# Performance work log

Measured on AMD Instinct MI355X. Metric: run time of the kernel, lower is better.

The kernel has to match this reference:

```python
import jax, jax.numpy as jnp
import numpy as np

T, B, S = 32, 32, 64
I = H = C = 1024  # input_size == hidden_size required by the original module's wiring
A = 128           # attention_size


def setup_inputs() -> dict:
    key = jax.random.key(0)
    ks = jax.random.split(key, 10)
    s_ih = 1.0 / np.sqrt(H)
    s_a = 1.0 / np.sqrt(H + C)
    return {
        "inputs": jax.random.normal(ks[0], (T, B, I), jnp.float32),
        "context": jax.random.normal(ks[1], (S, B, C), jnp.float32),
        # LSTMCell params (PyTorch layout: gates ordered i, f, g, o)
        "W_ih": jax.random.normal(ks[2], (4 * H, I), jnp.float32) * s_ih,
        "W_hh": jax.random.normal(ks[3], (4 * H, H), jnp.float32) * s_ih,
        "b_ih": jax.random.normal(ks[4], (4 * H,), jnp.float32) * s_ih,
        "b_hh": jax.random.normal(ks[5], (4 * H,), jnp.float32) * s_ih,
        # Attention params: linear1 [A, H+C], linear2 [1, A]
        "W1": jax.random.normal(ks[6], (A, H + C), jnp.float32) * s_a,
        "b1": jax.random.normal(ks[7], (A,), jnp.float32) * s_a,
        "W2": jax.random.normal(ks[8], (1, A), jnp.float32) * (1.0 / np.sqrt(A)),
        "b2": jax.random.normal(ks[9], (1,), jnp.float32) * (1.0 / np.sqrt(A)),
    }


def reference(inputs, context, W_ih, W_hh, b_ih, b_hh, W1, b1, W2, b2):
    Tn, Bn, _ = inputs.shape
    Hn = W_hh.shape[1]
    xt = jnp.transpose(context, (1, 0, 2))  # [B, S, C]
    # Split linear1 weight into hidden-part and context-part so the
    # context projection can be hoisted out of the time loop (same math
    # as concatenating [y, xt] then applying linear1).
    W1_y = W1[:, :Hn]          # [A, H]
    W1_x = W1[:, Hn:]          # [A, C]
    ctx_proj = jnp.einsum('bsc,ac->bsa', xt, W1_x)  # [B, S, A]
    bias = b_ih + b_hh

    def step(carry, x_t):
        h, c = carry
        gates = x_t @ W_ih.T + h @ W_hh.T + bias   # [B, 4H]
        i, f, g, o = jnp.split(gates, 4, axis=-1)
        c_new = jax.nn.sigmoid(f) * c + jax.nn.sigmoid(i) * jnp.tanh(g)
        h_new = jax.nn.sigmoid(o) * jnp.tanh(c_new)
        # additive attention: linear1 (no nonlinearity in original) -> linear2 -> softmax
        hid = h_new[:, None, :] @ W1_y.T[None] + ctx_proj + b1  # [B, S, A]
        scores = jnp.einsum('bsa,a->bs', hid, W2[0]) + b2[0]    # [B, S]
        attn = jax.nn.softmax(scores, axis=-1)
        weighted = jnp.einsum('bs,bsc->bc', attn, xt)           # [B, C]
        return (h_new, c_new), (weighted, attn)

    h0 = jnp.zeros((Bn, Hn), inputs.dtype)
    (h, c), (outputs, attentions) = jax.lax.scan(step, (h0, h0), inputs)
    return outputs, h, c, attentions
```

## Files before the change

kernel.cpp:

```cpp
#include <hip/hip_runtime.h>

#define T_ 32
#define B_ 32
#define S_ 64
#define C_ 1024
#define H_ 1024
#define NWG 64
#define HSLOT 32768

typedef __attribute__((ext_vector_type(8))) short bf16x8;
typedef __attribute__((ext_vector_type(4))) float f32x4;

#define OUT_H   1048576
#define OUT_CC  1081344
#define OUT_AT  1114112

__device__ __forceinline__ ushort f2b(float f) {
  unsigned u = __float_as_uint(f);
  unsigned r = (u + 0x7FFFu + ((u >> 16) & 1u)) >> 16;
  return (ushort)r;
}
__device__ __forceinline__ float b2f(ushort h) {
  return __uint_as_float(((unsigned)h) << 16);
}

__global__ __launch_bounds__(256) void k_init(const float* __restrict__ inp, ushort* __restrict__ inpb,
                                              const float* __restrict__ Wih, ushort* __restrict__ Wihb,
                                              const float* __restrict__ Whh, ushort* __restrict__ Whhb,
                                              const float* __restrict__ W1, const float* __restrict__ W2,
                                              const float* __restrict__ bih, const float* __restrict__ bhh,
                                              float* __restrict__ v, float* __restrict__ bias,
                                              ushort* __restrict__ hring, unsigned* __restrict__ flags) {
  int blk = blockIdx.x, tid = threadIdx.x;
  if (blk < 4608) {
    const float* src; ushort* dst; int base;
    if (blk < 512) { src = inp; dst = inpb; base = blk; }
    else if (blk < 2560) { src = Wih; dst = Wihb; base = blk - 512; }
    else { src = Whh; dst = Whhb; base = blk - 2560; }
    size_t i = ((size_t)base * 256 + tid) * 8;
    float4 v0 = *reinterpret_cast<const float4*>(src + i);
    float4 v1 = *reinterpret_cast<const float4*>(src + i + 4);
    uint4 o;
    o.x = (unsigned)f2b(v0.x) | ((unsigned)f2b(v0.y) << 16);
    o.y = (unsigned)f2b(v0.z) | ((unsigned)f2b(v0.w) << 16);
    o.z = (unsigned)f2b(v1.x) | ((unsigned)f2b(v1.y) << 16);
    o.w = (unsigned)f2b(v1.z) | ((unsigned)f2b(v1.w) << 16);
    *reinterpret_cast<uint4*>(dst + i) = o;
  } else if (blk < 4612) {
    int c = (blk - 4608) * 256 + tid;
    float acc = 0.f;
#pragma unroll 8
    for (int a = 0; a < 128; ++a) acc += W1[a * 2048 + 1024 + c] * W2[a];
    v[c] = acc;
  } else if (blk < 4628) {
    int jj = (blk - 4612) * 256 + tid;
    bias[jj] = bih[jj] + bhh[jj];
  } else if (blk < 4632) {
    unsigned* hz = reinterpret_cast<unsigned*>(hring);
    int base = (blk - 4628) * 4096;
    for (int i = 0; i < 16; ++i) hz[base + i * 256 + tid] = 0u;
  } else {
    for (int i = 0; i < 4; ++i) flags[i * 256 + tid] = 0u;
  }
}

__global__ __launch_bounds__(256) void k_attn(const float* __restrict__ ctx, const float* __restrict__ v,
                                              float* __restrict__ wgt, float* __restrict__ out) {
  int b = blockIdx.x, tid = threadIdx.x;
  int lane = tid & 63, w = tid >> 6;
  __shared__ float v_s[1024];
  __shared__ float sc_s[64];
  __shared__ float att_s[64];
  for (int i = 0; i < 4; ++i) v_s[tid + i * 256] = v[tid + i * 256];
  __syncthreads();
  for (int si = 0; si < 16; ++si) {
    int s = w * 16 + si;
    const float* xr = ctx + (size_t)(s * B_ + b) * C_;
    float acc = 0.f;
#pragma unroll
    for (int i = 0; i < 16; ++i) { int c = lane + i * 64; acc += xr[c] * v_s[c]; }
    for (int off = 32; off; off >>= 1) acc += __shfl_down(acc, off);
    if (lane == 0) sc_s[s] = acc;
  }
  __syncthreads();
  if (tid < 64) {
    float val = sc_s[tid];
    float mx = val;
    for (int off = 32; off; off >>= 1) mx = fmaxf(mx, __shfl_xor(mx, off));
    float e = expf(val - mx);
    float sm = e;
    for (int off = 32; off; off >>= 1) sm += __shfl_xor(sm, off);
    att_s[tid] = e / sm;
  }
  __syncthreads();
  const float4* ctx4 = reinterpret_cast<const float4*>(ctx);
  float4 a4 = {0.f, 0.f, 0.f, 0.f};
  for (int s = 0; s < 64; ++s) {
    float a = att_s[s];
    float4 x = ctx4[(size_t)(s * B_ + b) * 256 + tid];
    a4.x += a * x.x; a4.y += a * x.y; a4.z += a * x.z; a4.w += a * x.w;
  }
  reinterpret_cast<float4*>(wgt + b * 1024)[tid] = a4;
  if (tid < 64) {
    float av = att_s[tid];
#pragma unroll 4
    for (int t = 0; t < T_; ++t) out[OUT_AT + (t * B_ + b) * 64 + tid] = av;
  }
}

__global__ __launch_bounds__(1024, 4) void k_rec(const ushort* __restrict__ Whhb, const ushort* __restrict__ Wihb,
                                                 const ushort* __restrict__ inpb, ushort* __restrict__ hring,
                                                 const float* __restrict__ wgt, const float* __restrict__ bias,
                                                 float* __restrict__ out, unsigned* __restrict__ flags) {
  int tid = threadIdx.x, lane = tid & 63, w = tid >> 6;
  int wg = blockIdx.x;
  int q = w & 3, ks = w >> 2;
  int g = lane >> 4, r = lane & 15;
  int hidx0 = wg * 16 + q * 4;
  int kbase = ks * 256;
  int j = (r >> 2) * 1024 + hidx0 + (r & 3);
  bf16x8 ah[8], ax[8];
  {
    const ushort* ap = Whhb + (size_t)j * 1024 + kbase + g * 8;
    const ushort* axp = Wihb + (size_t)j * 1024 + kbase + g * 8;
#pragma unroll
    for (int kk = 0; kk < 8; ++kk) {
      ah[kk] = *reinterpret_cast<const bf16x8*>(ap + kk * 32);
      ax[kk] = *reinterpret_cast<const bf16x8*>(axp + kk * 32);
    }
  }
  __shared__ uint4 hl4[4096];
  __shared__ float red[4][4][16][32];
  __shared__ __align__(16) ushort hs[32][16];
  float c_reg = 0.f;
  int eb = tid & 31, hl = (tid >> 5) & 3, qq = tid >> 7;
  int ehidx = wg * 16 + qq * 4 + hl;
  float bs_i = 0.f, bs_f = 0.f, bs_g = 0.f, bs_o = 0.f;
  if (tid < 512) {
    bs_i = bias[ehidx];
    bs_f = bias[1024 + ehidx];
    bs_g = bias[2048 + ehidx];
    bs_o = bias[3072 + ehidx];
  }
  int cb = ks * 32 + g;

#pragma unroll 1
  for (int t = 0; t < T_; ++t) {
    {
      const uint4* s4 = reinterpret_cast<const uint4*>(inpb + (size_t)t * HSLOT);
      uint4 v0 = s4[tid], v1 = s4[tid + 1024], v2 = s4[tid + 2048], v3 = s4[tid + 3072];
      int c0 = tid, c1 = tid + 1024, c2 = tid + 2048, c3 = tid + 3072;
      hl4[(c0 >> 7) * 128 + ((c0 & 127) ^ ((c0 >> 7) & 7))] = v0;
      hl4[(c1 >> 7) * 128 + ((c1 & 127) ^ ((c1 >> 7) & 7))] = v1;
      hl4[(c2 >> 7) * 128 + ((c2 & 127) ^ ((c2 >> 7) & 7))] = v2;
      hl4[(c3 >> 7) * 128 + ((c3 & 127) ^ ((c3 >> 7) & 7))] = v3;
    }
    __syncthreads();
    f32x4 acc0 = (f32x4)(0.f), acc1 = (f32x4)(0.f);
#pragma unroll
    for (int kk = 0; kk < 8; ++kk) {
      int c16 = cb + kk * 4;
      bf16x8 b0 = *reinterpret_cast<const bf16x8*>(&hl4[r * 128 + (c16 ^ (r & 7))]);
      bf16x8 b1 = *reinterpret_cast<const bf16x8*>(&hl4[(r + 16) * 128 + (c16 ^ (r & 7))]);
      acc0 = __builtin_amdgcn_mfma_f32_16x16x32_bf16(ax[kk], b0, acc0, 0, 0, 0);
      acc1 = __builtin_amdgcn_mfma_f32_16x16x32_bf16(ax[kk], b1, acc1, 0, 0, 0);
    }
    if (t > 0 && w == 0) {
      for (;;) {
        unsigned vfl = __hip_atomic_load(&flags[lane * 16], __ATOMIC_RELAXED, __HIP_MEMORY_SCOPE_AGENT);
        if (__all((int)(vfl >= (unsigned)t))) break;
        __builtin_amdgcn_s_sleep(1);
      }
    }
    __syncthreads();
    {
      const uint4* s4 = reinterpret_cast<const uint4*>(hring + (size_t)t * HSLOT);
      uint4 v0 = s4[tid], v1 = s4[tid + 1024], v2 = s4[tid + 2048], v3 = s4[tid + 3072];
      int c0 = tid, c1 = tid + 1024, c2 = tid + 2048, c3 = tid + 3072;
      hl4[(c0 >> 7) * 128 + ((c0 & 127) ^ ((c0 >> 7) & 7))] = v0;
      hl4[(c1 >> 7) * 128 + ((c1 & 127) ^ ((c1 >> 7) & 7))] = v1;
      hl4[(c2 >> 7) * 128 + ((c2 & 127) ^ ((c2 >> 7) & 7))] = v2;
      hl4[(c3 >> 7) * 128 + ((c3 & 127) ^ ((c3 >> 7) & 7))] = v3;
    }
    __syncthreads();
#pragma unroll
    for (int kk = 0; kk < 8; ++kk) {
      int c16 = cb + kk * 4;
      bf16x8 b0 = *reinterpret_cast<const bf16x8*>(&hl4[r * 128 + (c16 ^ (r & 7))]);
      bf16x8 b1 = *reinterpret_cast<const bf16x8*>(&hl4[(r + 16) * 128 + (c16 ^ (r & 7))]);
      acc0 = __builtin_amdgcn_mfma_f32_16x16x32_bf16(ah[kk], b0, acc0, 0, 0, 0);
      acc1 = __builtin_amdgcn_mfma_f32_16x16x32_bf16(ah[kk], b1, acc1, 0, 0, 0);
    }
#pragma unroll
    for (int e = 0; e < 4; ++e) {
      red[q][ks][g * 4 + e][r] = acc0[e];
      red[q][ks][g * 4 + e][r + 16] = acc1[e];
    }
    __syncthreads();
    if (tid < 512) {
      float ig = red[qq][0][0 + hl][eb]  + red[qq][1][0 + hl][eb]  + red[qq][2][0 + hl][eb]  + red[qq][3][0 + hl][eb]  + bs_i;
      float fg = red[qq][0][4 + hl][eb]  + red[qq][1][4 + hl][eb]  + red[qq][2][4 + hl][eb]  + red[qq][3][4 + hl][eb]  + bs_f;
      float gg = red[qq][0][8 + hl][eb]  + red[qq][1][8 + hl][eb]  + red[qq][2][8 + hl][eb]  + red[qq][3][8 + hl][eb]  + bs_g;
      float og = red[qq][0][12 + hl][eb] + red[qq][1][12 + hl][eb] + red[qq][2][12 + hl][eb] + red[qq][3][12 + hl][eb] + bs_o;
      float si = 1.f / (1.f + __expf(-ig));
      float sf = 1.f / (1.f + __expf(-fg));
      float so = 1.f / (1.f + __expf(-og));
      float c_new = sf * c_reg + si * tanhf(gg);
      float h_new = so * tanhf(c_new);
      c_reg = c_new;
      hs[eb][qq * 4 + hl] = f2b(h_new);
      if (t == T_ - 1) {
        out[OUT_H + eb * 1024 + ehidx] = h_new;
        out[OUT_CC + eb * 1024 + ehidx] = c_new;
      }
    }
    __syncthreads();
    if (t != T_ - 1 && w == 0) {
      ushort* hout = hring + (size_t)(t + 1) * HSLOT;
      int b = lane >> 1, half = lane & 1;
      uint4 vv = *reinterpret_cast<const uint4*>(&hs[b][half * 8]);
      unsigned* hp = reinterpret_cast<unsigned*>(hout) + b * 512 + wg * 8 + half * 4;
      __hip_atomic_store(hp + 0, vv.x, __ATOMIC_RELAXED, __HIP_MEMORY_SCOPE_AGENT);
      __hip_atomic_store(hp + 1, vv.y, __ATOMIC_RELAXED, __HIP_MEMORY_SCOPE_AGENT);
      __hip_atomic_store(hp + 2, vv.z, __ATOMIC_RELAXED, __HIP_MEMORY_SCOPE_AGENT);
      __hip_atomic_store(hp + 3, vv.w, __ATOMIC_RELAXED, __HIP_MEMORY_SCOPE_AGENT);
      asm volatile("s_waitcnt vmcnt(0)" ::: "memory");
      if (lane == 0)
        __hip_atomic_store(&flags[wg * 16], (unsigned)(t + 1), __ATOMIC_RELAXED, __HIP_MEMORY_SCOPE_AGENT);
    }
    if (tid >= 512 && tid < 640) {
      int lcl = tid - 512;
      int off = ((wg & 1) << 9) + (lcl << 2);
      float4 vv = *reinterpret_cast<const float4*>(wgt + ((wg >> 1) << 10) + off);
      *reinterpret_cast<float4*>(out + ((size_t)(t * 32 + (wg >> 1)) << 10) + off) = vv;
    }
  }
}

extern "C" void kernel_launch(void* const* d_in, const int* in_sizes, int n_in,
                              void* d_out, int out_size, void* d_ws, size_t ws_size,
                              hipStream_t stream) {
  const float* inp = (const float*)d_in[0];
  const float* ctx = (const float*)d_in[1];
  const float* Wih = (const float*)d_in[2];
  const float* Whh = (const float*)d_in[3];
  const float* bih = (const float*)d_in[4];
  const float* bhh = (const float*)d_in[5];
  const float* W1  = (const float*)d_in[6];
  const float* W2  = (const float*)d_in[8];
  float* out = (float*)d_out;
  char* wsb = (char*)d_ws;

  float* v     = (float*)(wsb + 0);
  float* bias  = (float*)(wsb + 4096);
  float* wgt   = (float*)(wsb + 20480);
  ushort* hring = (ushort*)(wsb + 151552);
  ushort* inpb = (ushort*)(wsb + 2314240);
  ushort* Wihb = (ushort*)(wsb + 4411392);
  ushort* Whhb = (ushort*)(wsb + 12800000);
  unsigned* flags = (unsigned*)(wsb + 21188608);

  hipLaunchKernelGGL(k_init, dim3(4633), dim3(256), 0, stream,
                     inp, inpb, Wih, Wihb, Whh, Whhb, W1, W2, bih, bhh, v, bias, hring, flags);
  hipLaunchKernelGGL(k_attn, dim3(32), dim3(256), 0, stream, ctx, v, wgt, out);

  const ushort* Whhb_c = Whhb;
  const ushort* Wihb_c = Wihb;
  const ushort* inpb_c = inpb;
  const float* wgt_c = wgt;
  const float* bias_c = bias;
  void* kargs[8];
  kargs[0] = (void*)&Whhb_c;
  kargs[1] = (void*)&Wihb_c;
  kargs[2] = (void*)&inpb_c;
  kargs[3] = (void*)&hring;
  kargs[4] = (void*)&wgt_c;
  kargs[5] = (void*)&bias_c;
  kargs[6] = (void*)&out;
  kargs[7] = (void*)&flags;
  hipLaunchCooperativeKernel((const void*)k_rec, dim3(NWG), dim3(1024), kargs, 0, stream);
}
```

Measured before the change: 217.7 us.

## Fuse input and recurrent GEMMs via concatenated weights, LDS atomic reduction

Concatenates W_ih and W_hh into one [4H, 2H] bf16 matrix so each wave does a single K=512 MFMA chain over [x_t, h_t] staged together in LDS. The split-K reduction now uses LDS atomicAdd into a double-buffered accumulator instead of summing four partials. The weighted-context output is written for every timestep directly by the attention kernel instead of by the recurrent kernel. The cost is that the x_t @ W_ih product, which used to run before the spin-wait and overlap it, now sits on the critical path after the barrier. The change also adds LDS atomic contention and uses twice the LDS buffer.

```diff
diff --git a/kernel.cpp b/kernel.cpp
--- a/kernel.cpp
+++ b/kernel.cpp
@@ -25,19 +25,29 @@
 }
 
 __global__ __launch_bounds__(256) void k_init(const float* __restrict__ inp, ushort* __restrict__ inpb,
-                                              const float* __restrict__ Wih, ushort* __restrict__ Wihb,
-                                              const float* __restrict__ Whh, ushort* __restrict__ Whhb,
+                                              const float* __restrict__ Wih, const float* __restrict__ Whh,
+                                              ushort* __restrict__ Wcat,
                                               const float* __restrict__ W1, const float* __restrict__ W2,
                                               const float* __restrict__ bih, const float* __restrict__ bhh,
                                               float* __restrict__ v, float* __restrict__ bias,
                                               ushort* __restrict__ hring, unsigned* __restrict__ flags) {
   int blk = blockIdx.x, tid = threadIdx.x;
-  if (blk < 4608) {
-    const float* src; ushort* dst; int base;
-    if (blk < 512) { src = inp; dst = inpb; base = blk; }
-    else if (blk < 2560) { src = Wih; dst = Wihb; base = blk - 512; }
-    else { src = Whh; dst = Whhb; base = blk - 2560; }
+  if (blk < 512) {
+    size_t i = ((size_t)blk * 256 + tid) * 8;
+    float4 v0 = *reinterpret_cast<const float4*>(inp + i);
+    float4 v1 = *reinterpret_cast<const float4*>(inp + i + 4);
+    uint4 o;
+    o.x = (unsigned)f2b(v0.x) | ((unsigned)f2b(v0.y) << 16);
+    o.y = (unsigned)f2b(v0.z) | ((unsigned)f2b(v0.w) << 16);
+    o.z = (unsigned)f2b(v1.x) | ((unsigned)f2b(v1.y) << 16);
+    o.w = (unsigned)f2b(v1.z) | ((unsigned)f2b(v1.w) << 16);
+    *reinterpret_cast<uint4*>(inpb + i) = o;
+  } else if (blk < 4608) {
+    const float* src = (blk < 2560) ? Wih : Whh;
+    int base = (blk < 2560) ? (blk - 512) : (blk - 2560);
+    int koff = (blk < 2560) ? 0 : 1024;
     size_t i = ((size_t)base * 256 + tid) * 8;
+    int j = (int)(i >> 10), k = (int)(i & 1023);
     float4 v0 = *reinterpret_cast<const float4*>(src + i);
     float4 v1 = *reinterpret_cast<const float4*>(src + i + 4);
     uint4 o;
@@ -45,7 +55,7 @@
     o.y = (unsigned)f2b(v0.z) | ((unsigned)f2b(v0.w) << 16);
     o.z = (unsigned)f2b(v1.x) | ((unsigned)f2b(v1.y) << 16);
     o.w = (unsigned)f2b(v1.z) | ((unsigned)f2b(v1.w) << 16);
-    *reinterpret_cast<uint4*>(dst + i) = o;
+    *reinterpret_cast<uint4*>(Wcat + (size_t)j * 2048 + koff + k) = o;
   } else if (blk < 4612) {
     int c = (blk - 4608) * 256 + tid;
     float acc = 0.f;
@@ -65,7 +75,7 @@
 }
 
 __global__ __launch_bounds__(256) void k_attn(const float* __restrict__ ctx, const float* __restrict__ v,
-                                              float* __restrict__ wgt, float* __restrict__ out) {
+                                              float* __restrict__ out) {
   int b = blockIdx.x, tid = threadIdx.x;
   int lane = tid & 63, w = tid >> 6;
   __shared__ float v_s[1024];
@@ -100,7 +110,9 @@
     float4 x = ctx4[(size_t)(s * B_ + b) * 256 + tid];
     a4.x += a * x.x; a4.y += a * x.y; a4.z += a * x.z; a4.w += a * x.w;
   }
-  reinterpret_cast<float4*>(wgt + b * 1024)[tid] = a4;
+#pragma unroll 4
+  for (int t = 0; t < T_; ++t)
+    reinterpret_cast<float4*>(out + (size_t)(t * B_ + b) * C_)[tid] = a4;
   if (tid < 64) {
     float av = att_s[tid];
 #pragma unroll 4
@@ -108,29 +120,22 @@
   }
 }
 
-__global__ __launch_bounds__(1024, 4) void k_rec(const ushort* __restrict__ Whhb, const ushort* __restrict__ Wihb,
-                                                 const ushort* __restrict__ inpb, ushort* __restrict__ hring,
-                                                 const float* __restrict__ wgt, const float* __restrict__ bias,
+__global__ __launch_bounds__(1024, 4) void k_rec(const ushort* __restrict__ Wcat, const ushort* __restrict__ inpb,
+                                                 ushort* __restrict__ hring, const float* __restrict__ bias,
                                                  float* __restrict__ out, unsigned* __restrict__ flags) {
   int tid = threadIdx.x, lane = tid & 63, w = tid >> 6;
   int wg = blockIdx.x;
   int q = w & 3, ks = w >> 2;
   int g = lane >> 4, r = lane & 15;
-  int hidx0 = wg * 16 + q * 4;
-  int kbase = ks * 256;
-  int j = (r >> 2) * 1024 + hidx0 + (r & 3);
-  bf16x8 ah[8], ax[8];
+  int j = (r >> 2) * 1024 + wg * 16 + q * 4 + (r & 3);
+  bf16x8 a[16];
   {
-    const ushort* ap = Whhb + (size_t)j * 1024 + kbase + g * 8;
-    const ushort* axp = Wihb + (size_t)j * 1024 + kbase + g * 8;
-#pragma unroll
-    for (int kk = 0; kk < 8; ++kk) {
-      ah[kk] = *reinterpret_cast<const bf16x8*>(ap + kk * 32);
-      ax[kk] = *reinterpret_cast<const bf16x8*>(axp + kk * 32);
-    }
-  }
-  __shared__ uint4 hl4[4096];
-  __shared__ float red[4][4][16][32];
+    const ushort* ap = Wcat + (size_t)j * 2048 + ks * 512 + g * 8;
+#pragma unroll
+    for (int kk = 0; kk < 16; ++kk) a[kk] = *reinterpret_cast<const bf16x8*>(ap + kk * 32);
+  }
+  __shared__ uint4 buf[8192];
+  __shared__ float red[2][4][16][32];
   __shared__ __align__(16) ushort hs[32][16];
   float c_reg = 0.f;
   int eb = tid & 31, hl = (tid >> 5) & 3, qq = tid >> 7;
@@ -142,29 +147,17 @@
     bs_g = bias[2048 + ehidx];
     bs_o = bias[3072 + ehidx];
   }
-  int cb = ks * 32 + g;
+  int c16s = tid & 255, rowb = tid >> 8;
+  int swz_w[8];
+#pragma unroll
+  for (int i = 0; i < 8; ++i) {
+    int row = rowb + i * 4;
+    swz_w[i] = row * 256 + (c16s ^ (row & 7));
+  }
 
 #pragma unroll 1
   for (int t = 0; t < T_; ++t) {
-    {
-      const uint4* s4 = reinterpret_cast<const uint4*>(inpb + (size_t)t * HSLOT);
-      uint4 v0 = s4[tid], v1 = s4[tid + 1024], v2 = s4[tid + 2048], v3 = s4[tid + 3072];
-      int c0 = tid, c1 = tid + 1024, c2 = tid + 2048, c3 = tid + 3072;
-      hl4[(c0 >> 7) * 128 + ((c0 & 127) ^ ((c0 >> 7) & 7))] = v0;
-      hl4[(c1 >> 7) * 128 + ((c1 & 127) ^ ((c1 >> 7) & 7))] = v1;
-      hl4[(c2 >> 7) * 128 + ((c2 & 127) ^ ((c2 >> 7) & 7))] = v2;
-      hl4[(c3 >> 7) * 128 + ((c3 & 127) ^ ((c3 >> 7) & 7))] = v3;
-    }
-    __syncthreads();
-    f32x4 acc0 = (f32x4)(0.f), acc1 = (f32x4)(0.f);
-#pragma unroll
-    for (int kk = 0; kk < 8; ++kk) {
-      int c16 = cb + kk * 4;
-      bf16x8 b0 = *reinterpret_cast<const bf16x8*>(&hl4[r * 128 + (c16 ^ (r & 7))]);
-      bf16x8 b1 = *reinterpret_cast<const bf16x8*>(&hl4[(r + 16) * 128 + (c16 ^ (r & 7))]);
-      acc0 = __builtin_amdgcn_mfma_f32_16x16x32_bf16(ax[kk], b0, acc0, 0, 0, 0);
-      acc1 = __builtin_amdgcn_mfma_f32_16x16x32_bf16(ax[kk], b1, acc1, 0, 0, 0);
-    }
+    int p = t & 1;
     if (t > 0 && w == 0) {
       for (;;) {
         unsigned vfl = __hip_atomic_load(&flags[lane * 16], __ATOMIC_RELAXED, __HIP_MEMORY_SCOPE_AGENT);
@@ -174,34 +167,46 @@
     }
     __syncthreads();
     {
-      const uint4* s4 = reinterpret_cast<const uint4*>(hring + (size_t)t * HSLOT);
-      uint4 v0 = s4[tid], v1 = s4[tid + 1024], v2 = s4[tid + 2048], v3 = s4[tid + 3072];
-      int c0 = tid, c1 = tid + 1024, c2 = tid + 2048, c3 = tid + 3072;
-      hl4[(c0 >> 7) * 128 + ((c0 & 127) ^ ((c0 >> 7) & 7))] = v0;
-      hl4[(c1 >> 7) * 128 + ((c1 & 127) ^ ((c1 >> 7) & 7))] = v1;
-      hl4[(c2 >> 7) * 128 + ((c2 & 127) ^ ((c2 >> 7) & 7))] = v2;
-      hl4[(c3 >> 7) * 128 + ((c3 & 127) ^ ((c3 >> 7) & 7))] = v3;
-    }
-    __syncthreads();
-#pragma unroll
-    for (int kk = 0; kk < 8; ++kk) {
+      float* z = &red[p ^ 1][0][0][0];
+      z[tid] = 0.f; z[tid + 1024] = 0.f;
+      if (t == 0) {
+        float* z0 = &red[0][0][0][0];
+        z0[tid] = 0.f; z0[tid + 1024] = 0.f;
+      }
+    }
+    {
+      const ushort* xsrc = inpb + (size_t)t * HSLOT;
+      const ushort* hsrc = hring + (size_t)t * HSLOT;
+      const ushort* colb = (c16s < 128) ? (xsrc + c16s * 8) : (hsrc + (c16s - 128) * 8);
+#pragma unroll
+      for (int i = 0; i < 8; ++i) {
+        int row = rowb + i * 4;
+        buf[swz_w[i]] = *reinterpret_cast<const uint4*>(colb + (size_t)row * 1024);
+      }
+    }
+    __syncthreads();
+    f32x4 acc0 = (f32x4)(0.f), acc1 = (f32x4)(0.f);
+    int cb = ks * 64 + g;
+#pragma unroll
+    for (int kk = 0; kk < 16; ++kk) {
       int c16 = cb + kk * 4;
-      bf16x8 b0 = *reinterpret_cast<const bf16x8*>(&hl4[r * 128 + (c16 ^ (r & 7))]);
-      bf16x8 b1 = *reinterpret_cast<const bf16x8*>(&hl4[(r + 16) * 128 + (c16 ^ (r & 7))]);
-      acc0 = __builtin_amdgcn_mfma_f32_16x16x32_bf16(ah[kk], b0, acc0, 0, 0, 0);
-      acc1 = __builtin_amdgcn_mfma_f32_16x16x32_bf16(ah[kk], b1, acc1, 0, 0, 0);
+      int x0 = r * 256 + (c16 ^ (r & 7));
+      bf16x8 b0 = *reinterpret_cast<const bf16x8*>(&buf[x0]);
+      bf16x8 b1 = *reinterpret_cast<const bf16x8*>(&buf[x0 + 16 * 256]);
+      acc0 = __builtin_amdgcn_mfma_f32_16x16x32_bf16(a[kk], b0, acc0, 0, 0, 0);
+      acc1 = __builtin_amdgcn_mfma_f32_16x16x32_bf16(a[kk], b1, acc1, 0, 0, 0);
     }
 #pragma unroll
     for (int e = 0; e < 4; ++e) {
-      red[q][ks][g * 4 + e][r] = acc0[e];
-      red[q][ks][g * 4 + e][r + 16] = acc1[e];
+      atomicAdd(&red[p][q][g * 4 + e][r], acc0[e]);
+      atomicAdd(&red[p][q][g * 4 + e][r + 16], acc1[e]);
     }
     __syncthreads();
     if (tid < 512) {
-      float ig = red[qq][0][0 + hl][eb]  + red[qq][1][0 + hl][eb]  + red[qq][2][0 + hl][eb]  + red[qq][3][0 + hl][eb]  + bs_i;
-      float fg = red[qq][0][4 + hl][eb]  + red[qq][1][4 + hl][eb]  + red[qq][2][4 + hl][eb]  + red[qq][3][4 + hl][eb]  + bs_f;
-      float gg = red[qq][0][8 + hl][eb]  + red[qq][1][8 + hl][eb]  + red[qq][2][8 + hl][eb]  + red[qq][3][8 + hl][eb]  + bs_g;
-      float og = red[qq][0][12 + hl][eb] + red[qq][1][12 + hl][eb] + red[qq][2][12 + hl][eb] + red[qq][3][12 + hl][eb] + bs_o;
+      float ig = red[p][qq][0 + hl][eb]  + bs_i;
+      float fg = red[p][qq][4 + hl][eb]  + bs_f;
+      float gg = red[p][qq][8 + hl][eb]  + bs_g;
+      float og = red[p][qq][12 + hl][eb] + bs_o;
       float si = 1.f / (1.f + __expf(-ig));
       float sf = 1.f / (1.f + __expf(-fg));
       float so = 1.f / (1.f + __expf(-og));
@@ -227,12 +232,6 @@
       asm volatile("s_waitcnt vmcnt(0)" ::: "memory");
       if (lane == 0)
         __hip_atomic_store(&flags[wg * 16], (unsigned)(t + 1), __ATOMIC_RELAXED, __HIP_MEMORY_SCOPE_AGENT);
-    }
-    if (tid >= 512 && tid < 640) {
-      int lcl = tid - 512;
-      int off = ((wg & 1) << 9) + (lcl << 2);
-      float4 vv = *reinterpret_cast<const float4*>(wgt + ((wg >> 1) << 10) + off);
-      *reinterpret_cast<float4*>(out + ((size_t)(t * 32 + (wg >> 1)) << 10) + off) = vv;
     }
   }
 }
@@ -253,30 +252,24 @@
 
   float* v     = (float*)(wsb + 0);
   float* bias  = (float*)(wsb + 4096);
-  float* wgt   = (float*)(wsb + 20480);
-  ushort* hring = (ushort*)(wsb + 151552);
-  ushort* inpb = (ushort*)(wsb + 2314240);
-  ushort* Wihb = (ushort*)(wsb + 4411392);
-  ushort* Whhb = (ushort*)(wsb + 12800000);
-  unsigned* flags = (unsigned*)(wsb + 21188608);
+  ushort* hring = (ushort*)(wsb + 32768);
+  ushort* inpb = (ushort*)(wsb + 2195456);
+  ushort* Wcat = (ushort*)(wsb + 4292608);
+  unsigned* flags = (unsigned*)(wsb + 21069824);
 
   hipLaunchKernelGGL(k_init, dim3(4633), dim3(256), 0, stream,
-                     inp, inpb, Wih, Wihb, Whh, Whhb, W1, W2, bih, bhh, v, bias, hring, flags);
-  hipLaunchKernelGGL(k_attn, dim3(32), dim3(256), 0, stream, ctx, v, wgt, out);
-
-  const ushort* Whhb_c = Whhb;
-  const ushort* Wihb_c = Wihb;
+                     inp, inpb, Wih, Whh, Wcat, W1, W2, bih, bhh, v, bias, hring, flags);
+  hipLaunchKernelGGL(k_attn, dim3(32), dim3(256), 0, stream, ctx, v, out);
+
+  const ushort* Wcat_c = Wcat;
   const ushort* inpb_c = inpb;
-  const float* wgt_c = wgt;
   const float* bias_c = bias;
-  void* kargs[8];
-  kargs[0] = (void*)&Whhb_c;
-  kargs[1] = (void*)&Wihb_c;
-  kargs[2] = (void*)&inpb_c;
-  kargs[3] = (void*)&hring;
-  kargs[4] = (void*)&wgt_c;
-  kargs[5] = (void*)&bias_c;
-  kargs[6] = (void*)&out;
-  kargs[7] = (void*)&flags;
+  void* kargs[6];
+  kargs[0] = (void*)&Wcat_c;
+  kargs[1] = (void*)&inpb_c;
+  kargs[2] = (void*)&hring;
+  kargs[3] = (void*)&bias_c;
+  kargs[4] = (void*)&out;
+  kargs[5] = (void*)&flags;
   hipLaunchCooperativeKernel((const void*)k_rec, dim3(NWG), dim3(1024), kargs, 0, stream);
 }
```

New measurement: 593.8 us. +172.7%, slower.

## Fuse attention kernel into cooperative recurrent kernel as extra workgroups

Applied to the files above, without the earlier changes.

Removes the separate attention launch by adding 32 extra workgroups to the cooperative recurrent kernel that compute the attention scores, softmax and weighted context per batch and write outputs directly for all timesteps. The recurrent workgroups no longer copy the weighted vector into the output each step. This saves one kernel launch and runs attention concurrently with the recurrence. In exchange it adds more LDS per block and more workgroups that must be co-resident for the cooperative launch.

```diff
diff --git a/kernel.cpp b/kernel.cpp
--- a/kernel.cpp
+++ b/kernel.cpp
@@ -64,56 +64,68 @@
   }
 }
 
-__global__ __launch_bounds__(256) void k_attn(const float* __restrict__ ctx, const float* __restrict__ v,
-                                              float* __restrict__ wgt, float* __restrict__ out) {
-  int b = blockIdx.x, tid = threadIdx.x;
-  int lane = tid & 63, w = tid >> 6;
+__global__ __launch_bounds__(1024, 4) void k_rec(const ushort* __restrict__ Whhb, const ushort* __restrict__ Wihb,
+                                                 const ushort* __restrict__ inpb, ushort* __restrict__ hring,
+                                                 const float* __restrict__ ctx, const float* __restrict__ v,
+                                                 const float* __restrict__ bias,
+                                                 float* __restrict__ out, unsigned* __restrict__ flags) {
+  int tid = threadIdx.x, lane = tid & 63, w = tid >> 6;
+  int wg = blockIdx.x;
+
+  __shared__ uint4 hl4[4096];
+  __shared__ float red[4][4][16][32];
+  __shared__ __align__(16) ushort hs[32][16];
   __shared__ float v_s[1024];
   __shared__ float sc_s[64];
   __shared__ float att_s[64];
-  for (int i = 0; i < 4; ++i) v_s[tid + i * 256] = v[tid + i * 256];
-  __syncthreads();
-  for (int si = 0; si < 16; ++si) {
-    int s = w * 16 + si;
-    const float* xr = ctx + (size_t)(s * B_ + b) * C_;
-    float acc = 0.f;
-#pragma unroll
-    for (int i = 0; i < 16; ++i) { int c = lane + i * 64; acc += xr[c] * v_s[c]; }
-    for (int off = 32; off; off >>= 1) acc += __shfl_down(acc, off);
-    if (lane == 0) sc_s[s] = acc;
-  }
-  __syncthreads();
-  if (tid < 64) {
-    float val = sc_s[tid];
-    float mx = val;
-    for (int off = 32; off; off >>= 1) mx = fmaxf(mx, __shfl_xor(mx, off));
-    float e = expf(val - mx);
-    float sm = e;
-    for (int off = 32; off; off >>= 1) sm += __shfl_xor(sm, off);
-    att_s[tid] = e / sm;
-  }
-  __syncthreads();
-  const float4* ctx4 = reinterpret_cast<const float4*>(ctx);
-  float4 a4 = {0.f, 0.f, 0.f, 0.f};
-  for (int s = 0; s < 64; ++s) {
-    float a = att_s[s];
-    float4 x = ctx4[(size_t)(s * B_ + b) * 256 + tid];
-    a4.x += a * x.x; a4.y += a * x.y; a4.z += a * x.z; a4.w += a * x.w;
-  }
-  reinterpret_cast<float4*>(wgt + b * 1024)[tid] = a4;
-  if (tid < 64) {
-    float av = att_s[tid];
+
+  if (wg >= NWG) {
+    int b = wg - NWG;
+    v_s[tid] = v[tid];
+    __syncthreads();
+    {
+      int s = w * 4;
+#pragma unroll
+      for (int si = 0; si < 4; ++si, ++s) {
+        const float* xr = ctx + (size_t)(s * B_ + b) * C_;
+        float acc = 0.f;
+#pragma unroll
+        for (int i = 0; i < 16; ++i) { int c = lane + i * 64; acc += xr[c] * v_s[c]; }
+        for (int off = 32; off; off >>= 1) acc += __shfl_down(acc, off);
+        if (lane == 0) sc_s[s] = acc;
+      }
+    }
+    __syncthreads();
+    if (tid < 64) {
+      float val = sc_s[tid];
+      float mx = val;
+      for (int off = 32; off; off >>= 1) mx = fmaxf(mx, __shfl_xor(mx, off));
+      float e = expf(val - mx);
+      float sm = e;
+      for (int off = 32; off; off >>= 1) sm += __shfl_xor(sm, off);
+      att_s[tid] = e / sm;
+    }
+    __syncthreads();
+    if (tid < 256) {
+      const float4* ctx4 = reinterpret_cast<const float4*>(ctx);
+      float4 a4 = {0.f, 0.f, 0.f, 0.f};
+      for (int s = 0; s < 64; ++s) {
+        float a = att_s[s];
+        float4 x = ctx4[(size_t)(s * B_ + b) * 256 + tid];
+        a4.x += a * x.x; a4.y += a * x.y; a4.z += a * x.z; a4.w += a * x.w;
+      }
 #pragma unroll 4
-    for (int t = 0; t < T_; ++t) out[OUT_AT + (t * B_ + b) * 64 + tid] = av;
-  }
-}
-
-__global__ __launch_bounds__(1024, 4) void k_rec(const ushort* __restrict__ Whhb, const ushort* __restrict__ Wihb,
-                                                 const ushort* __restrict__ inpb, ushort* __restrict__ hring,
-                                                 const float* __restrict__ wgt, const float* __restrict__ bias,
-                                                 float* __restrict__ out, unsigned* __restrict__ flags) {
-  int tid = threadIdx.x, lane = tid & 63, w = tid >> 6;
-  int wg = blockIdx.x;
+      for (int t = 0; t < T_; ++t)
+        reinterpret_cast<float4*>(out + (size_t)(t * B_ + b) * C_)[tid] = a4;
+    }
+    if (tid < 64) {
+      float av = att_s[tid];
+#pragma unroll 4
+      for (int t = 0; t < T_; ++t) out[OUT_AT + (t * B_ + b) * 64 + tid] = av;
+    }
+    return;
+  }
+
   int q = w & 3, ks = w >> 2;
   int g = lane >> 4, r = lane & 15;
   int hidx0 = wg * 16 + q * 4;
@@ -129,9 +141,6 @@
       ax[kk] = *reinterpret_cast<const bf16x8*>(axp + kk * 32);
     }
   }
-  __shared__ uint4 hl4[4096];
-  __shared__ float red[4][4][16][32];
-  __shared__ __align__(16) ushort hs[32][16];
   float c_reg = 0.f;
   int eb = tid & 31, hl = (tid >> 5) & 3, qq = tid >> 7;
   int ehidx = wg * 16 + qq * 4 + hl;
@@ -228,12 +237,6 @@
       if (lane == 0)
         __hip_atomic_store(&flags[wg * 16], (unsigned)(t + 1), __ATOMIC_RELAXED, __HIP_MEMORY_SCOPE_AGENT);
     }
-    if (tid >= 512 && tid < 640) {
-      int lcl = tid - 512;
-      int off = ((wg & 1) << 9) + (lcl << 2);
-      float4 vv = *reinterpret_cast<const float4*>(wgt + ((wg >> 1) << 10) + off);
-      *reinterpret_cast<float4*>(out + ((size_t)(t * 32 + (wg >> 1)) << 10) + off) = vv;
-    }
   }
 }
 
@@ -253,30 +256,30 @@
 
   float* v     = (float*)(wsb + 0);
   float* bias  = (float*)(wsb + 4096);
-  float* wgt   = (float*)(wsb + 20480);
-  ushort* hring = (ushort*)(wsb + 151552);
-  ushort* inpb = (ushort*)(wsb + 2314240);
-  ushort* Wihb = (ushort*)(wsb + 4411392);
-  ushort* Whhb = (ushort*)(wsb + 12800000);
-  unsigned* flags = (unsigned*)(wsb + 21188608);
+  ushort* hring = (ushort*)(wsb + 32768);
+  ushort* inpb = (ushort*)(wsb + 2195456);
+  ushort* Wihb = (ushort*)(wsb + 4292608);
+  ushort* Whhb = (ushort*)(wsb + 12681216);
+  unsigned* flags = (unsigned*)(wsb + 21069824);
 
   hipLaunchKernelGGL(k_init, dim3(4633), dim3(256), 0, stream,
                      inp, inpb, Wih, Wihb, Whh, Whhb, W1, W2, bih, bhh, v, bias, hring, flags);
-  hipLaunchKernelGGL(k_attn, dim3(32), dim3(256), 0, stream, ctx, v, wgt, out);
 
   const ushort* Whhb_c = Whhb;
   const ushort* Wihb_c = Wihb;
   const ushort* inpb_c = inpb;
-  const float* wgt_c = wgt;
+  const float* ctx_c = ctx;
+  const float* v_c = v;
   const float* bias_c = bias;
-  void* kargs[8];
+  void* kargs[9];
   kargs[0] = (void*)&Whhb_c;
   kargs[1] = (void*)&Wihb_c;
   kargs[2] = (void*)&inpb_c;
   kargs[3] = (void*)&hring;
-  kargs[4] = (void*)&wgt_c;
-  kargs[5] = (void*)&bias_c;
-  kargs[6] = (void*)&out;
-  kargs[7] = (void*)&flags;
-  hipLaunchCooperativeKernel((const void*)k_rec, dim3(NWG), dim3(1024), kargs, 0, stream);
-}
+  kargs[4] = (void*)&ctx_c;
+  kargs[5] = (void*)&v_c;
+  kargs[6] = (void*)&bias_c;
+  kargs[7] = (void*)&out;
+  kargs[8] = (void*)&flags;
+  hipLaunchCooperativeKernel((const void*)k_rec, dim3(NWG + 32), dim3(1024), kargs, 0, stream);
+}
```

After: 198.0 us, median of 2. 9.1% less time.
